# Kernel tuning notes

Measured on AMD Instinct MI355X. Metric: run time of the kernel, lower is better.

Reference implementation:

```python
import jax, jax.numpy as jnp
import numpy as np

N_NODES = 50000


def setup_inputs() -> dict:
    key = jax.random.key(0)
    ks = jax.random.split(key, 6)
    S, E, F = 4, 800000, 128
    feat = jax.random.normal(ks[0], (N_NODES, F), dtype=jnp.float32)
    src = jax.random.randint(ks[1], (S, E), 0, N_NODES, dtype=jnp.int64)
    dst = jax.random.randint(ks[2], (S, E), 0, N_NODES, dtype=jnp.int64)
    # torch Linear(2F, F) weight used as x @ W here: shape [2F, F]
    W_attn = jax.random.normal(ks[3], (S, 2 * F, F), dtype=jnp.float32) * 0.05
    b_attn = jnp.zeros((S, F), dtype=jnp.float32)
    w_out = jax.random.normal(ks[4], (S, F), dtype=jnp.float32) * 0.05
    return {"feat": feat, "src": src, "dst": dst,
            "W_attn": W_attn, "b_attn": b_attn, "w_out": w_out}


def _space_conv(feat, srck, dstk, W, b, w, n):
    # edge attention: tanh(attn_fc([h_src || h_dst])) @ attn_out
    h_src = feat[srck]                                   # [E, F] gather
    h_dst = feat[dstk]                                   # [E, F] gather
    hc = jnp.concatenate([h_src, h_dst], axis=1)         # [E, 2F]
    e = jnp.tanh(hc @ W + b) @ w                         # [E]
    # segment softmax over incoming edges of each dst node
    m = jax.ops.segment_max(e, dstk, num_segments=n)     # [N]
    ex = jnp.exp(e - m[dstk])
    s = jax.ops.segment_sum(ex, dstk, num_segments=n)    # [N]
    alpha = ex / s[dstk]                                 # [E]
    # weighted scatter-sum of (untransformed) src features
    return jax.ops.segment_sum(alpha[:, None] * h_src, dstk, num_segments=n)  # [N, F]


def reference(feat, src, dst, W_attn, b_attn, w_out):
    n = feat.shape[0]
    S = src.shape[0]
    # sequential over the small fixed number of angle spaces keeps peak memory low
    h_list = [_space_conv(feat, src[k], dst[k], W_attn[k], b_attn[k], w_out[k], n)
              for k in range(S)]
    return jnp.concatenate(h_list, axis=-1)              # merge='cat' -> [N, S*F]
```

## Files before the change

### kernel.cpp

```cpp
#include <hip/hip_runtime.h>
#include <hip/hip_bf16.h>


#define F 128

typedef __attribute__((ext_vector_type(8))) short short8v;
typedef __attribute__((ext_vector_type(4))) float f32x4;
typedef __attribute__((ext_vector_type(2))) float f32x2;

__device__ __forceinline__ unsigned f2bf(float x) {
    unsigned u = __float_as_uint(x);
    unsigned r = ((u >> 16) & 1u) + 0x7fffu;
    return (u + r) >> 16;
}
__device__ __forceinline__ float bf_lo(unsigned v) { return __uint_as_float(v << 16); }
__device__ __forceinline__ float bf_hi(unsigned v) { return __uint_as_float(v & 0xffff0000u); }

__global__ __launch_bounds__(256) void cvt_feat_kernel(
    const float* __restrict__ feat, unsigned* __restrict__ feat16, int n4)
{
    for (int i = blockIdx.x * 256 + threadIdx.x; i < n4; i += gridDim.x * 256) {
        float4 v = *(const float4*)(feat + (size_t)i * 4);
        unsigned lo = f2bf(v.x) | (f2bf(v.y) << 16);
        unsigned hi = f2bf(v.z) | (f2bf(v.w) << 16);
        *(uint2*)(feat16 + (size_t)i * 2) = make_uint2(lo, hi);
    }
}

__global__ __launch_bounds__(256) void cvt_w_kernel(
    const float* __restrict__ W, unsigned short* __restrict__ Wt, int total)
{
    int tid = blockIdx.x * 256 + threadIdx.x;
    if (tid >= total) return;
    int i = tid & 127;
    int c = (tid >> 7) & 255;
    int s = tid >> 15;
    float v = W[(size_t)s * 32768 + (size_t)(((c >> 7) << 7) + i) * 128 + (c & 127)];
    Wt[tid] = (unsigned short)f2bf(v);
}

__global__ __launch_bounds__(256) void proj_mfma_kernel(
    const unsigned short* __restrict__ feat16s,
    const unsigned short* __restrict__ WtAll,
    const float* __restrict__ bvec,
    unsigned char* __restrict__ a8, unsigned short* __restrict__ bp16s,
    int N, int k0)
{
    __shared__ uint4 wlds4[4096];
    const int t = threadIdx.x;
    const int w = t >> 6, l = t & 63;
    const int by = blockIdx.y, k = k0 + by;
    const int row0 = blockIdx.x * 64 + w * 16;
    const unsigned short* Wk = WtAll + (size_t)k * 256 * 128;

    {
        const uint4* Wg = (const uint4*)Wk;
        char* wb = (char*)wlds4;
        for (int i = t; i < 4096; i += 256) {
            int c = i >> 4;
            int swz = (i * 16) ^ ((c & 7) << 4);
            *(uint4*)(wb + swz) = Wg[i];
        }
    }
    __syncthreads();

    const int lrow = l & 15;
    const int rs = l >> 4;
    const int lk = rs * 8;

    f32x4 acc[16];
    #pragma unroll
    for (int jt = 0; jt < 16; ++jt) acc[jt] = (f32x4){0.f, 0.f, 0.f, 0.f};

    const int arow = row0 + lrow;
    const bool aok = arow < N;
    const unsigned short* ap = feat16s + (size_t)arow * 128 + lk;
    const char* wb = (const char*)wlds4;

    #pragma unroll
    for (int kk = 0; kk < 4; ++kk) {
        short8v af = {0, 0, 0, 0, 0, 0, 0, 0};
        if (aok) af = *(const short8v*)(ap + kk * 32);
        #pragma unroll
        for (int jt = 0; jt < 16; ++jt) {
            int c = jt * 16 + lrow;
            int byte = (c * 256 + kk * 64 + rs * 16) ^ ((c & 7) << 4);
            short8v bf = *(const short8v*)(wb + byte);
            acc[jt] = __builtin_amdgcn_mfma_f32_16x16x32_bf16(af, bf, acc[jt], 0, 0, 0);
        }
    }

    unsigned char*  a8k   = a8    + (size_t)by * N * 128;
    unsigned short* bp16k = bp16s + (size_t)by * N * 128;

    float bias[8];
    #pragma unroll
    for (int i = 0; i < 8; ++i) bias[i] = bvec[(size_t)k * F + i * 16 + lrow];

    #pragma unroll
    for (int r = 0; r < 4; ++r) {
        int node = row0 + rs * 4 + r;
        if (node >= N) continue;
        int w0i = __builtin_amdgcn_cvt_pk_fp8_f32(acc[0][r], acc[1][r], 0, false);
        w0i = __builtin_amdgcn_cvt_pk_fp8_f32(acc[2][r], acc[3][r], w0i, true);
        int w1i = __builtin_amdgcn_cvt_pk_fp8_f32(acc[4][r], acc[5][r], 0, false);
        w1i = __builtin_amdgcn_cvt_pk_fp8_f32(acc[6][r], acc[7][r], w1i, true);
        *(uint2*)(a8k + (size_t)node * 128 + lrow * 8) =
            make_uint2((unsigned)w0i, (unsigned)w1i);
        uint4 o;
        o.x = f2bf(acc[8][r]  + bias[0]) | (f2bf(acc[9][r]  + bias[1]) << 16);
        o.y = f2bf(acc[10][r] + bias[2]) | (f2bf(acc[11][r] + bias[3]) << 16);
        o.z = f2bf(acc[12][r] + bias[4]) | (f2bf(acc[13][r] + bias[5]) << 16);
        o.w = f2bf(acc[14][r] + bias[6]) | (f2bf(acc[15][r] + bias[7]) << 16);
        *(uint4*)(bp16k + (size_t)node * 128 + lrow * 8) = o;
    }
}

__global__ __launch_bounds__(256) void bucket_count_kernel(
    const int* __restrict__ dst, int* __restrict__ bkt_cnt,
    int E, int SE, int NB, int NBS)
{
    __shared__ int hist[1024];
    const int t = threadIdx.x;
    for (int i = t; i < NBS; i += 256) hist[i] = 0;
    __syncthreads();
    const int chunk = (SE + gridDim.x - 1) / gridDim.x;
    const int e0 = blockIdx.x * chunk;
    const int e1 = min(SE, e0 + chunk);
    for (int e = e0 + t; e < e1; e += 256) {
        int s = e / E;
        atomicAdd(&hist[s * NB + (dst[e] >> 8)], 1);
    }
    __syncthreads();
    for (int i = t; i < NBS; i += 256)
        if (hist[i]) atomicAdd(&bkt_cnt[i], hist[i]);
}

__global__ __launch_bounds__(1024) void bucket_scan_kernel(
    const int* __restrict__ bkt_cnt, int* __restrict__ bkt_off,
    int* __restrict__ bkt_cur, int NBS)
{
    __shared__ int buf[1024];
    const int t = threadIdx.x;
    buf[t] = (t < NBS) ? bkt_cnt[t] : 0;
    __syncthreads();
    for (int off = 1; off < 1024; off <<= 1) {
        int x = (t >= off) ? buf[t - off] : 0;
        __syncthreads();
        buf[t] += x;
        __syncthreads();
    }
    if (t <= NBS) {
        int v = (t == 0) ? 0 : buf[t - 1];
        bkt_off[t] = v;
        if (t < NBS) bkt_cur[t] = v;
    }
}

__global__ __launch_bounds__(256) void bucket_scatter_kernel(
    const int* __restrict__ src, const int* __restrict__ dst,
    int* __restrict__ bkt_cur, unsigned* __restrict__ recs,
    int E, int SE, int NB, int NBS)
{
    __shared__ int hist[1024];
    __shared__ int base[1024];
    const int t = threadIdx.x;
    for (int i = t; i < NBS; i += 256) hist[i] = 0;
    __syncthreads();
    const int chunk = (SE + gridDim.x - 1) / gridDim.x;
    const int e0 = blockIdx.x * chunk;
    const int e1 = min(SE, e0 + chunk);
    for (int e = e0 + t; e < e1; e += 256) {
        int s = e / E;
        atomicAdd(&hist[s * NB + (dst[e] >> 8)], 1);
    }
    __syncthreads();
    for (int i = t; i < NBS; i += 256) {
        int h = hist[i];
        if (h) base[i] = atomicAdd(&bkt_cur[i], h);
        hist[i] = 0;
    }
    __syncthreads();
    for (int e = e0 + t; e < e1; e += 256) {
        int s = e / E;
        int d = dst[e];
        int gb = s * NB + (d >> 8);
        int lo = atomicAdd(&hist[gb], 1);
        recs[base[gb] + lo] = (unsigned)src[e] | ((unsigned)(d & 255) << 16);
    }
}

__global__ __launch_bounds__(256) void node_count_bucket_kernel(
    const unsigned* __restrict__ recs, const int* __restrict__ bkt_off,
    int* __restrict__ cnt, int N, int NB)
{
    __shared__ int hist[256];
    const int t = threadIdx.x;
    const int gb = blockIdx.x;
    const int s = gb / NB;
    const int node0 = (gb % NB) << 8;
    hist[t] = 0;
    __syncthreads();
    const int r0 = bkt_off[gb], r1 = bkt_off[gb + 1];
    for (int r = r0 + t; r < r1; r += 256)
        atomicAdd(&hist[(recs[r] >> 16) & 255], 1);
    __syncthreads();
    int node = node0 + t;
    if (node < N) cnt[(size_t)s * N + node] = hist[t];
}

__global__ __launch_bounds__(256) void partial_kernel(
    const int* __restrict__ cnt, int* __restrict__ partials, int N, int BPS)
{
    __shared__ int red[256];
    const int s = blockIdx.y, b = blockIdx.x, t = threadIdx.x;
    int i = b * 256 + t;
    red[t] = (i < N) ? cnt[(size_t)s * N + i] : 0;
    __syncthreads();
    #pragma unroll
    for (int off = 128; off; off >>= 1) {
        if (t < off) red[t] += red[t + off];
        __syncthreads();
    }
    if (t == 0) partials[s * BPS + b] = red[0];
}

__global__ __launch_bounds__(1024) void scan_partials_kernel(
    const int* __restrict__ partials, int* __restrict__ scanned,
    int* __restrict__ row_off, int S, int BPS, int N)
{
    __shared__ int buf[1024];
    const int t = threadIdx.x;
    const int total = S * BPS;
    buf[t] = (t < total) ? partials[t] : 0;
    __syncthreads();
    for (int off = 1; off < 1024; off <<= 1) {
        int x = (t >= off) ? buf[t - off] : 0;
        __syncthreads();
        buf[t] += x;
        __syncthreads();
    }
    if (t < total) {
        int s = t / BPS;
        int g_excl = (t == 0) ? 0 : buf[t - 1];
        int base = (s == 0) ? 0 : buf[s * BPS - 1];
        scanned[t] = g_excl - base;
    }
    if (t < S) {
        int end  = buf[(t + 1) * BPS - 1];
        int base = (t == 0) ? 0 : buf[t * BPS - 1];
        row_off[(size_t)t * (N + 1) + N] = end - base;
    }
}

__global__ __launch_bounds__(256) void emit_kernel(
    const int* __restrict__ cnt, const int* __restrict__ scanned,
    int* __restrict__ row_off, int N, int BPS)
{
    __shared__ int buf[256];
    const int s = blockIdx.y, b = blockIdx.x, t = threadIdx.x;
    int i = b * 256 + t;
    int v = (i < N) ? cnt[(size_t)s * N + i] : 0;
    buf[t] = v;
    __syncthreads();
    for (int off = 1; off < 256; off <<= 1) {
        int x = (t >= off) ? buf[t - off] : 0;
        __syncthreads();
        buf[t] += x;
        __syncthreads();
    }
    if (i < N)
        row_off[(size_t)s * (N + 1) + i] = scanned[s * BPS + b] + buf[t] - v;
}

__global__ __launch_bounds__(256) void csr_fill_bucket_kernel(
    const unsigned* __restrict__ recs, const int* __restrict__ bkt_off,
    const int* __restrict__ row_off, int* __restrict__ src_csr,
    int N, int E, int NB)
{
    __shared__ int cur[256];
    const int t = threadIdx.x;
    const int gb = blockIdx.x;
    const int s = gb / NB;
    const int node0 = (gb % NB) << 8;
    int node = node0 + t;
    cur[t] = (node < N) ? row_off[(size_t)s * (N + 1) + node] : 0;
    __syncthreads();
    int* csr = src_csr + (size_t)s * E;
    const int r0 = bkt_off[gb], r1 = bkt_off[gb + 1];
    for (int r = r0 + t; r < r1; r += 256) {
        unsigned rec = recs[r];
        int pos = atomicAdd(&cur[(rec >> 16) & 255], 1);
        csr[pos] = (int)(rec & 0xFFFFu);
    }
}

__global__ __launch_bounds__(256) void count_all_kernel(
    const int* __restrict__ dst, int* __restrict__ cnt, int E, int SE, int N)
{
    int e = blockIdx.x * 256 + threadIdx.x;
    if (e < SE) {
        int s = e / E;
        atomicAdd(&cnt[(size_t)s * N + dst[e]], 1);
    }
}
__global__ __launch_bounds__(256) void emit_cursor_kernel(
    const int* __restrict__ row_off, int* __restrict__ cursor, int N)
{
    const int s = blockIdx.y;
    int i = blockIdx.x * 256 + threadIdx.x;
    if (i < N) cursor[(size_t)s * N + i] = row_off[(size_t)s * (N + 1) + i];
}
__global__ __launch_bounds__(256) void fill_all_kernel(
    const int* __restrict__ src, const int* __restrict__ dst,
    int* __restrict__ cursor, int* __restrict__ src_csr,
    int E, int SE, int N)
{
    int e = blockIdx.x * 256 + threadIdx.x;
    if (e < SE) {
        int s = e / E;
        int pos = atomicAdd(&cursor[(size_t)s * N + dst[e]], 1);
        src_csr[(size_t)s * E + pos] = src[e];
    }
}

__global__ __launch_bounds__(256) void fused_kernel(
    const uint4* __restrict__ feat16, const uint2* __restrict__ a8,
    const uint4* __restrict__ bp16, const float* __restrict__ wout,
    const int* __restrict__ src_csr_all, const int* __restrict__ row_off_all,
    float* __restrict__ out, int N, int S, int E, int k0)
{
    const int by = blockIdx.y, k = k0 + by;
    const int wslot = threadIdx.x >> 6;
    const int node = blockIdx.x * 4 + wslot;
    const int lane = threadIdx.x & 63;
    const int eg = lane >> 4;
    const int fl = lane & 15;
    if (node >= N) return;

    const int* row_off = row_off_all + (size_t)k * (N + 1);
    const int* src_csr = src_csr_all + (size_t)k * E;
    const uint2* a8k  = a8   + (size_t)by * N * 16;
    const uint4* bp16k = bp16 + (size_t)by * N * 16;

    const int beg = row_off[node];
    const int cnt = row_off[node + 1] - beg;
    float* outp = out + (size_t)node * (S * F) + k * F;
    if (cnt == 0) {
        if (eg == 0) {
            *(float4*)(outp + fl * 8)     = make_float4(0.f, 0.f, 0.f, 0.f);
            *(float4*)(outp + fl * 8 + 4) = make_float4(0.f, 0.f, 0.f, 0.f);
        }
        return;
    }

    const float C2  = 2.8853900817779268f;
    const float L2E = 1.4426950408889634f;

    uint4 bv = bp16k[(size_t)node * 16 + fl];
    float bc[8];
    bc[0] = bf_lo(bv.x) * C2; bc[1] = bf_hi(bv.x) * C2;
    bc[2] = bf_lo(bv.y) * C2; bc[3] = bf_hi(bv.y) * C2;
    bc[4] = bf_lo(bv.z) * C2; bc[5] = bf_hi(bv.z) * C2;
    bc[6] = bf_lo(bv.w) * C2; bc[7] = bf_hi(bv.w) * C2;
    const float* wk = wout + (size_t)k * F;
    float wv[8];
    #pragma unroll
    for (int i = 0; i < 8; ++i) wv[i] = wk[i * 16 + fl];

    float sumw = 0.f, sabs = 0.f;
    #pragma unroll
    for (int i = 0; i < 8; ++i) { sumw += wv[i]; sabs += fabsf(wv[i]); }
    #pragma unroll
    for (int off = 1; off < 16; off <<= 1) {
        sumw += __shfl_xor(sumw, off);
        sabs += __shfl_xor(sabs, off);
    }
    const float negswl = -sabs * L2E;

    float ssum = 0.f;
    float acc[8] = {0.f, 0.f, 0.f, 0.f, 0.f, 0.f, 0.f, 0.f};
    for (int chunk = 0; chunk < cnt; chunk += 64) {
        int idx = chunk + lane;
        int sv = (idx < cnt) ? src_csr[beg + idx] : 0;
        int cend = min(64, cnt - chunk);
        for (int q = 0; q < cend; q += 4) {
            int my = q + eg;
            int sj = __shfl(sv, my);
            uint2 av8 = a8k[(size_t)sj * 16 + fl];
            uint4 fv  = feat16[(size_t)sj * 16 + fl];
            f32x2 a01 = __builtin_amdgcn_cvt_pk_f32_fp8(av8.x, false);
            f32x2 a23 = __builtin_amdgcn_cvt_pk_f32_fp8(av8.x, true);
            f32x2 a45 = __builtin_amdgcn_cvt_pk_f32_fp8(av8.y, false);
            f32x2 a67 = __builtin_amdgcn_cvt_pk_f32_fp8(av8.y, true);
            float pr;
            pr  = wv[0] * __builtin_amdgcn_rcpf(__builtin_exp2f(fmaf(a01.x, C2, bc[0])) + 1.f);
            pr += wv[1] * __builtin_amdgcn_rcpf(__builtin_exp2f(fmaf(a01.y, C2, bc[1])) + 1.f);
            pr += wv[2] * __builtin_amdgcn_rcpf(__builtin_exp2f(fmaf(a23.x, C2, bc[2])) + 1.f);
            pr += wv[3] * __builtin_amdgcn_rcpf(__builtin_exp2f(fmaf(a23.y, C2, bc[3])) + 1.f);
            pr += wv[4] * __builtin_amdgcn_rcpf(__builtin_exp2f(fmaf(a45.x, C2, bc[4])) + 1.f);
            pr += wv[5] * __builtin_amdgcn_rcpf(__builtin_exp2f(fmaf(a45.y, C2, bc[5])) + 1.f);
            pr += wv[6] * __builtin_amdgcn_rcpf(__builtin_exp2f(fmaf(a67.x, C2, bc[6])) + 1.f);
            pr += wv[7] * __builtin_amdgcn_rcpf(__builtin_exp2f(fmaf(a67.y, C2, bc[7])) + 1.f);
            pr += __shfl_xor(pr, 1);
            pr += __shfl_xor(pr, 2);
            pr += __shfl_xor(pr, 4);
            pr += __shfl_xor(pr, 8);
            float p = sumw - 2.f * pr;
            float ex = (my < cend) ? __builtin_exp2f(fmaf(p, L2E, negswl)) : 0.f;
            ssum += ex;
            acc[0] = fmaf(ex, bf_lo(fv.x), acc[0]);
            acc[1] = fmaf(ex, bf_hi(fv.x), acc[1]);
            acc[2] = fmaf(ex, bf_lo(fv.y), acc[2]);
            acc[3] = fmaf(ex, bf_hi(fv.y), acc[3]);
            acc[4] = fmaf(ex, bf_lo(fv.z), acc[4]);
            acc[5] = fmaf(ex, bf_hi(fv.z), acc[5]);
            acc[6] = fmaf(ex, bf_lo(fv.w), acc[6]);
            acc[7] = fmaf(ex, bf_hi(fv.w), acc[7]);
        }
    }
    ssum += __shfl_xor(ssum, 16);
    ssum += __shfl_xor(ssum, 32);
    #pragma unroll
    for (int j = 0; j < 8; ++j) {
        acc[j] += __shfl_xor(acc[j], 16);
        acc[j] += __shfl_xor(acc[j], 32);
    }
    float inv = __builtin_amdgcn_rcpf(ssum);
    if (eg == 0) {
        *(float4*)(outp + fl * 8) =
            make_float4(acc[0] * inv, acc[1] * inv, acc[2] * inv, acc[3] * inv);
        *(float4*)(outp + fl * 8 + 4) =
            make_float4(acc[4] * inv, acc[5] * inv, acc[6] * inv, acc[7] * inv);
    }
}

extern "C" void kernel_launch(void* const* d_in, const int* in_sizes, int n_in,
                              void* d_out, int out_size, void* d_ws, size_t ws_size,
                              hipStream_t stream) {
    const float* feat = (const float*)d_in[0];
    const int*   src  = (const int*)d_in[1];
    const int*   dst  = (const int*)d_in[2];
    const float* W    = (const float*)d_in[3];
    const float* bvec = (const float*)d_in[4];
    const float* wout = (const float*)d_in[5];
    float* out = (float*)d_out;

    const int N = in_sizes[0] / F;
    const int S = in_sizes[3] / (2 * F * F);
    const int E = in_sizes[1] / S;
    const int SE = S * E;
    const int BPS = (N + 255) / 256;
    const int NB  = (N + 255) >> 8;
    const int NBS = NB * S;
    const bool packed = (N <= 65536) && (NBS <= 1024) && (S * BPS <= 1024);

    size_t fixed = (size_t)N * 256
                 + (size_t)S * 32768 * 2
                 + (size_t)SE * 4
                 + (size_t)SE * 4
                 + (size_t)S * N * 4
                 + (size_t)S * (N + 1) * 4
                 + (size_t)S * BPS * 4 * 2
                 + (size_t)(NBS + 1) * 4 * 3;
    size_t perB = (size_t)N * 128
                + (size_t)N * 256;
    const int B = (ws_size >= fixed + perB * (size_t)S + 1024) ? S : 1;

    char* p = (char*)d_ws;
    unsigned* feat16     = (unsigned*)p;        p += (size_t)N * 256;
    unsigned char* a8    = (unsigned char*)p;   p += (size_t)B * N * 128;
    unsigned short* bp16 = (unsigned short*)p;  p += (size_t)B * N * 256;
    unsigned short* Wt   = (unsigned short*)p;  p += (size_t)S * 32768 * 2;
    int*      src_csr  = (int*)p;               p += (size_t)SE * 4;
    unsigned* recs     = (unsigned*)p;          p += (size_t)SE * 4;
    int*      cnt      = (int*)p;               p += (size_t)S * N * 4;
    int*      row_off  = (int*)p;               p += (size_t)S * (N + 1) * 4;
    int*      partials = (int*)p;               p += (size_t)S * BPS * 4;
    int*      scanned  = (int*)p;               p += (size_t)S * BPS * 4;
    int*      bkt_cnt  = (int*)p;               p += (size_t)(NBS + 1) * 4;
    int*      bkt_off  = (int*)p;               p += (size_t)(NBS + 1) * 4;
    int*      bkt_cur  = (int*)p;

    const int n4 = N * F / 4;
    const int proj_blocks = (N + 63) / 64;
    const int node_blocks = (N + 3) / 4;
    const int se_blocks   = (SE + 255) / 256;
    const int wt_total    = S * 256 * 128;

    cvt_feat_kernel<<<2048, 256, 0, stream>>>(feat, feat16, n4);
    cvt_w_kernel<<<(wt_total + 255) / 256, 256, 0, stream>>>(W, Wt, wt_total);

    if (packed) {
        hipMemsetAsync(bkt_cnt, 0, (size_t)NBS * sizeof(int), stream);
        bucket_count_kernel<<<512, 256, 0, stream>>>(dst, bkt_cnt, E, SE, NB, NBS);
        bucket_scan_kernel<<<1, 1024, 0, stream>>>(bkt_cnt, bkt_off, bkt_cur, NBS);
        bucket_scatter_kernel<<<512, 256, 0, stream>>>(src, dst, bkt_cur, recs,
                                                       E, SE, NB, NBS);
        node_count_bucket_kernel<<<NBS, 256, 0, stream>>>(recs, bkt_off, cnt, N, NB);
        partial_kernel<<<dim3(BPS, S), 256, 0, stream>>>(cnt, partials, N, BPS);
        scan_partials_kernel<<<1, 1024, 0, stream>>>(partials, scanned, row_off,
                                                     S, BPS, N);
        emit_kernel<<<dim3(BPS, S), 256, 0, stream>>>(cnt, scanned, row_off, N, BPS);
        csr_fill_bucket_kernel<<<NBS, 256, 0, stream>>>(recs, bkt_off, row_off,
                                                        src_csr, N, E, NB);
    } else {
        hipMemsetAsync(cnt, 0, (size_t)S * N * sizeof(int), stream);
        count_all_kernel<<<se_blocks, 256, 0, stream>>>(dst, cnt, E, SE, N);
        partial_kernel<<<dim3(BPS, S), 256, 0, stream>>>(cnt, partials, N, BPS);
        scan_partials_kernel<<<1, 1024, 0, stream>>>(partials, scanned, row_off,
                                                     S, BPS, N);
        emit_kernel<<<dim3(BPS, S), 256, 0, stream>>>(cnt, scanned, row_off, N, BPS);
        emit_cursor_kernel<<<dim3(BPS, S), 256, 0, stream>>>(row_off, cnt, N);
        fill_all_kernel<<<se_blocks, 256, 0, stream>>>(src, dst, cnt, src_csr,
                                                       E, SE, N);
    }

    for (int k0 = 0; k0 < S; k0 += B) {
        proj_mfma_kernel<<<dim3(proj_blocks, B), 256, 0, stream>>>(
            (const unsigned short*)feat16, Wt, bvec, a8, bp16, N, k0);
        fused_kernel<<<dim3(node_blocks, B), 256, 0, stream>>>(
            (const uint4*)feat16, (const uint2*)a8, (const uint4*)bp16, wout,
            src_csr, row_off, out, N, S, E, k0);
    }
}
```

Before: 368.1 us.

## Fuse per-bucket CSR construction into attention aggregation kernel using LDS

```diff
diff --git a/kernel.cpp b/kernel.cpp
--- a/kernel.cpp
+++ b/kernel.cpp
@@ -1,8 +1,10 @@
 #include <hip/hip_runtime.h>
 #include <hip/hip_bf16.h>
+#include <math.h>
 
 
 #define F 128
+#define CAPB 5632
 
 typedef __attribute__((ext_vector_type(8))) short short8v;
 typedef __attribute__((ext_vector_type(4))) float f32x4;
@@ -190,6 +192,161 @@
     }
 }
 
+__global__ __launch_bounds__(512) void fused_bucket_kernel(
+    const uint4* __restrict__ feat16, const uint2* __restrict__ a8,
+    const uint4* __restrict__ bp16, const float* __restrict__ wout,
+    const unsigned* __restrict__ recs, const int* __restrict__ bkt_off,
+    float* __restrict__ out, int N, int S, int NB)
+{
+    __shared__ int cnt_s[256];
+    __shared__ int off_s[256];
+    __shared__ int cur_s[256];
+    __shared__ unsigned short src_local[CAPB];
+
+    const int t = threadIdx.x;
+    const int gbid = blockIdx.x;
+    const int s = gbid % S;
+    const int bkt = gbid / S;
+    const int gb = s * NB + bkt;
+    const int node0 = bkt << 8;
+
+    if (t < 256) cnt_s[t] = 0;
+    __syncthreads();
+
+    const int r0 = bkt_off[gb], r1 = bkt_off[gb + 1];
+    for (int r = r0 + t; r < r1; r += 512)
+        atomicAdd(&cnt_s[(recs[r] >> 16) & 255], 1);
+    __syncthreads();
+
+    if (t < 256) off_s[t] = cnt_s[t];
+    __syncthreads();
+    for (int off = 1; off < 256; off <<= 1) {
+        int x = (t < 256 && t >= off) ? off_s[t - off] : 0;
+        __syncthreads();
+        if (t < 256) off_s[t] += x;
+        __syncthreads();
+    }
+    if (t < 256) cur_s[t] = off_s[t] - cnt_s[t];
+    __syncthreads();
+
+    for (int r = r0 + t; r < r1; r += 512) {
+        unsigned rec = recs[r];
+        int pos = atomicAdd(&cur_s[(rec >> 16) & 255], 1);
+        src_local[pos] = (unsigned short)(rec & 0xFFFFu);
+    }
+    __syncthreads();
+
+    const int wq = t >> 6;
+    const int lane = t & 63;
+    const int eg = lane >> 4;
+    const int fl = lane & 15;
+
+    const uint2* a8k   = a8   + (size_t)s * N * 16;
+    const uint4* bp16k = bp16 + (size_t)s * N * 16;
+
+    const float C2  = 2.8853900817779268f;
+    const float L2E = 1.4426950408889634f;
+
+    const float* wk = wout + (size_t)s * F;
+    float wv[8];
+    #pragma unroll
+    for (int i = 0; i < 8; ++i) wv[i] = wk[i * 16 + fl];
+    float sumw = 0.f, sabs = 0.f;
+    #pragma unroll
+    for (int i = 0; i < 8; ++i) { sumw += wv[i]; sabs += fabsf(wv[i]); }
+    #pragma unroll
+    for (int off = 1; off < 16; off <<= 1) {
+        sumw += __shfl_xor(sumw, off);
+        sabs += __shfl_xor(sabs, off);
+    }
+    const float negswl = -sabs * L2E;
+
+    for (int row = wq; row < 256; row += 8) {
+        const int node = node0 + row;
+        if (node >= N) break;
+        const int cnt = cnt_s[row];
+        float* outp = out + (size_t)node * (S * F) + s * F;
+        if (cnt == 0) {
+            if (eg == 0) {
+                *(float4*)(outp + fl * 8)     = make_float4(0.f, 0.f, 0.f, 0.f);
+                *(float4*)(outp + fl * 8 + 4) = make_float4(0.f, 0.f, 0.f, 0.f);
+            }
+            continue;
+        }
+        const int rbeg = off_s[row] - cnt;
+
+        uint4 bvv = bp16k[(size_t)node * 16 + fl];
+        float bc[8];
+        bc[0] = bf_lo(bvv.x) * C2; bc[1] = bf_hi(bvv.x) * C2;
+        bc[2] = bf_lo(bvv.y) * C2; bc[3] = bf_hi(bvv.y) * C2;
+        bc[4] = bf_lo(bvv.z) * C2; bc[5] = bf_hi(bvv.z) * C2;
+        bc[6] = bf_lo(bvv.w) * C2; bc[7] = bf_hi(bvv.w) * C2;
+
+        float ssum = 0.f;
+        float acc[8] = {0.f, 0.f, 0.f, 0.f, 0.f, 0.f, 0.f, 0.f};
+
+        int i0 = (eg < cnt) ? eg : (cnt - 1);
+        int sj = src_local[rbeg + i0];
+        uint2 av0 = a8k[(size_t)sj * 16 + fl];
+        uint4 fv0 = feat16[(size_t)sj * 16 + fl];
+
+        for (int q = 0; q < cnt; q += 4) {
+            uint2 av1; uint4 fv1;
+            const int qn = q + 4;
+            if (qn < cnt) {
+                int idx = qn + eg; if (idx >= cnt) idx = cnt - 1;
+                int sj1 = src_local[rbeg + idx];
+                av1 = a8k[(size_t)sj1 * 16 + fl];
+                fv1 = feat16[(size_t)sj1 * 16 + fl];
+            }
+            f32x2 a01 = __builtin_amdgcn_cvt_pk_f32_fp8(av0.x, false);
+            f32x2 a23 = __builtin_amdgcn_cvt_pk_f32_fp8(av0.x, true);
+            f32x2 a45 = __builtin_amdgcn_cvt_pk_f32_fp8(av0.y, false);
+            f32x2 a67 = __builtin_amdgcn_cvt_pk_f32_fp8(av0.y, true);
+            float pr;
+            pr  = wv[0] * __builtin_amdgcn_rcpf(__builtin_exp2f(fmaf(a01.x, C2, bc[0])) + 1.f);
+            pr += wv[1] * __builtin_amdgcn_rcpf(__builtin_exp2f(fmaf(a01.y, C2, bc[1])) + 1.f);
+            pr += wv[2] * __builtin_amdgcn_rcpf(__builtin_exp2f(fmaf(a23.x, C2, bc[2])) + 1.f);
+            pr += wv[3] * __builtin_amdgcn_rcpf(__builtin_exp2f(fmaf(a23.y, C2, bc[3])) + 1.f);
+            pr += wv[4] * __builtin_amdgcn_rcpf(__builtin_exp2f(fmaf(a45.x, C2, bc[4])) + 1.f);
+            pr += wv[5] * __builtin_amdgcn_rcpf(__builtin_exp2f(fmaf(a45.y, C2, bc[5])) + 1.f);
+            pr += wv[6] * __builtin_amdgcn_rcpf(__builtin_exp2f(fmaf(a67.x, C2, bc[6])) + 1.f);
+            pr += wv[7] * __builtin_amdgcn_rcpf(__builtin_exp2f(fmaf(a67.y, C2, bc[7])) + 1.f);
+            pr += __shfl_xor(pr, 1);
+            pr += __shfl_xor(pr, 2);
+            pr += __shfl_xor(pr, 4);
+            pr += __shfl_xor(pr, 8);
+            float p = sumw - 2.f * pr;
+            float ex = ((q + eg) < cnt) ? __builtin_exp2f(fmaf(p, L2E, negswl)) : 0.f;
+            ssum += ex;
+            acc[0] = fmaf(ex, bf_lo(fv0.x), acc[0]);
+            acc[1] = fmaf(ex, bf_hi(fv0.x), acc[1]);
+            acc[2] = fmaf(ex, bf_lo(fv0.y), acc[2]);
+            acc[3] = fmaf(ex, bf_hi(fv0.y), acc[3]);
+            acc[4] = fmaf(ex, bf_lo(fv0.z), acc[4]);
+            acc[5] = fmaf(ex, bf_hi(fv0.z), acc[5]);
+            acc[6] = fmaf(ex, bf_lo(fv0.w), acc[6]);
+            acc[7] = fmaf(ex, bf_hi(fv0.w), acc[7]);
+            av0 = av1;
+            fv0 = fv1;
+        }
+        ssum += __shfl_xor(ssum, 16);
+        ssum += __shfl_xor(ssum, 32);
+        #pragma unroll
+        for (int j = 0; j < 8; ++j) {
+            acc[j] += __shfl_xor(acc[j], 16);
+            acc[j] += __shfl_xor(acc[j], 32);
+        }
+        float inv = __builtin_amdgcn_rcpf(ssum);
+        if (eg == 0) {
+            *(float4*)(outp + fl * 8) =
+                make_float4(acc[0] * inv, acc[1] * inv, acc[2] * inv, acc[3] * inv);
+            *(float4*)(outp + fl * 8 + 4) =
+                make_float4(acc[4] * inv, acc[5] * inv, acc[6] * inv, acc[7] * inv);
+        }
+    }
+}
+
 __global__ __launch_bounds__(256) void node_count_bucket_kernel(
     const unsigned* __restrict__ recs, const int* __restrict__ bkt_off,
     int* __restrict__ cnt, int N, int NB)
@@ -331,8 +488,7 @@
     float* __restrict__ out, int N, int S, int E, int k0)
 {
     const int by = blockIdx.y, k = k0 + by;
-    const int wslot = threadIdx.x >> 6;
-    const int node = blockIdx.x * 4 + wslot;
+    const int node = blockIdx.x * 4 + (threadIdx.x >> 6);
     const int lane = threadIdx.x & 63;
     const int eg = lane >> 4;
     const int fl = lane & 15;
@@ -488,8 +644,26 @@
     const int se_blocks   = (SE + 255) / 256;
     const int wt_total    = S * 256 * 128;
 
+    const double avgb = (double)SE / (double)(NBS > 0 ? NBS : 1);
+    const bool bucketfused = packed && (B == S) &&
+        (avgb + 6.0 * sqrt(avgb) + 128.0 <= (double)CAPB);
+
     cvt_feat_kernel<<<2048, 256, 0, stream>>>(feat, feat16, n4);
     cvt_w_kernel<<<(wt_total + 255) / 256, 256, 0, stream>>>(W, Wt, wt_total);
+
+    if (bucketfused) {
+        hipMemsetAsync(bkt_cnt, 0, (size_t)NBS * sizeof(int), stream);
+        bucket_count_kernel<<<512, 256, 0, stream>>>(dst, bkt_cnt, E, SE, NB, NBS);
+        bucket_scan_kernel<<<1, 1024, 0, stream>>>(bkt_cnt, bkt_off, bkt_cur, NBS);
+        bucket_scatter_kernel<<<512, 256, 0, stream>>>(src, dst, bkt_cur, recs,
+                                                       E, SE, NB, NBS);
+        proj_mfma_kernel<<<dim3(proj_blocks, S), 256, 0, stream>>>(
+            (const unsigned short*)feat16, Wt, bvec, a8, bp16, N, 0);
+        fused_bucket_kernel<<<NB * S, 512, 0, stream>>>(
+            (const uint4*)feat16, (const uint2*)a8, (const uint4*)bp16, wout,
+            recs, bkt_off, out, N, S, NB);
+        return;
+    }
 
     if (packed) {
         hipMemsetAsync(bkt_cnt, 0, (size_t)NBS * sizeof(int), stream);
```

New measurement: 437.6 us. +18.9%, slower.
